# Optimization experiments

Measured on AMD Instinct MI355X. Metric: run time of the kernel, lower is better.

## Reference

```python
import jax, jax.numpy as jnp
import numpy as np

KS = 5          # kernel_size
D = 2           # spatial dim
DX = 0.01       # region kernel spacing
SCALE = 1.0
NX, NY = 32, 32
N = NX * NY


def _region_kernel():
    # gaussians.region_kernel: KS x KS grid of offsets spaced DX, centered at 0
    off = (jnp.arange(KS, dtype=jnp.float32) - (KS - 1) / 2.0) * DX
    gx, gy = jnp.meshgrid(off, off, indexing='ij')
    return jnp.stack([gx, gy], -1).reshape(-1, D)  # (KS*KS, 2)


def _build_cov(scaling, transform):
    # Cholesky-style parameterization: L lower-triangular with diag=scaling,
    # off-diag=transform; cov = L @ L^T (d=2 closed form)
    s0, s1 = scaling[:, 0], scaling[:, 1]
    t = transform[:, 0]
    c00 = s0 * s0
    c01 = s0 * t
    c11 = t * t + s1 * s1
    return jnp.stack([jnp.stack([c00, c01], -1), jnp.stack([c01, c11], -1)], -2)


def _inv2x2(c):
    det = c[:, 0, 0] * c[:, 1, 1] - c[:, 0, 1] * c[:, 1, 0]
    inv = jnp.stack([jnp.stack([c[:, 1, 1], -c[:, 0, 1]], -1),
                     jnp.stack([-c[:, 1, 0], c[:, 0, 0]], -1)], -2)
    return inv / det[:, None, None]


def setup_inputs() -> dict:
    key = jax.random.key(0)
    ks = jax.random.split(key, 20)
    # Gaussian state: grid means as in __init__
    tx = jnp.linspace(-1.0, 1.0, NX) * SCALE
    ty = jnp.linspace(-1.0, 1.0, NY) * SCALE
    gx, gy = jnp.meshgrid(tx, ty, indexing='ij')
    means = jnp.stack([gx, gy], -1).reshape(-1, D).astype(jnp.float32)
    u = 0.1 * jax.random.normal(ks[0], (N, 1), jnp.float32)
    scaling = jnp.exp(-4.5 + 0.2 * jax.random.normal(ks[1], (N, D), jnp.float32)) * SCALE
    transform = 0.002 * jax.random.normal(ks[2], (N, 1), jnp.float32)
    opacities = 2.0 + 0.1 * jax.random.normal(ks[3], (N,), jnp.float32)
    # network weights (4 heads share the first 3 layer shapes)
    convW = 0.05 * jax.random.normal(ks[4], (4, 50, 3, KS, KS), jnp.float32)
    convb = 0.01 * jax.random.normal(ks[5], (4, 50), jnp.float32)
    embW = 0.3 * jax.random.normal(ks[6], (4, 7, 30), jnp.float32)
    embb = 0.01 * jax.random.normal(ks[7], (4, 30), jnp.float32)
    l1W = 0.1 * jax.random.normal(ks[8], (4, 80, 80), jnp.float32)
    l1b = 0.01 * jax.random.normal(ks[9], (4, 80), jnp.float32)
    outW_sol = 0.1 * jax.random.normal(ks[10], (80, 1), jnp.float32)
    outb_sol = 0.01 * jax.random.normal(ks[11], (1,), jnp.float32)
    outW_trans = 0.1 * jax.random.normal(ks[12], (80, 2), jnp.float32)
    outb_trans = 0.01 * jax.random.normal(ks[13], (2,), jnp.float32)
    outW_scale = 0.1 * jax.random.normal(ks[14], (80, 2), jnp.float32)
    outb_scale = 0.01 * jax.random.normal(ks[15], (2,), jnp.float32)
    outW_tform = 0.1 * jax.random.normal(ks[16], (80, 1), jnp.float32)
    outb_tform = 0.01 * jax.random.normal(ks[17], (1,), jnp.float32)
    return {"means": means, "u": u, "scaling": scaling, "transform": transform,
            "opacities": opacities, "convW": convW, "convb": convb,
            "embW": embW, "embb": embb, "l1W": l1W, "l1b": l1b,
            "outW_sol": outW_sol, "outb_sol": outb_sol,
            "outW_trans": outW_trans, "outb_trans": outb_trans,
            "outW_scale": outW_scale, "outb_scale": outb_scale,
            "outW_tform": outW_tform, "outb_tform": outb_tform}


def reference(means, u, scaling, transform, opacities, convW, convb, embW, embb,
              l1W, l1b, outW_sol, outb_sol, outW_trans, outb_trans,
              outW_scale, outb_scale, outW_tform, outb_tform):
    n = means.shape[0]
    cov = _build_cov(scaling, transform)          # (N,2,2)
    conics = _inv2x2(cov)                         # (N,2,2)

    # --- sampling (torch.no_grad block in original) ---
    kern = _region_kernel()                                        # (25,2)
    samples = (means[:, None, :] + kern[None]).reshape(-1, D)      # (M,2), M=N*25
    bc = jnp.all(jnp.abs(samples) < SCALE, -1).astype(means.dtype)[:, None]
    alpha = jax.nn.sigmoid(opacities)                              # (N,)
    diff = samples[:, None, :] - means[None, :, :]                 # (M,N,2)
    Cq = jnp.einsum('nij,mnj->mni', conics, diff)                  # (M,N,2)
    G = jnp.exp(-0.5 * jnp.einsum('mni,mni->mn', diff, Cq)) * alpha[None, :]  # (M,N)
    u_s = G @ u                                                    # (M,1)
    # DIFFUSION pde_rhs = trace of laplacian: sum_n G * (|C q|^2 - tr(C)) * u_n
    trC = conics[:, 0, 0] + conics[:, 1, 1]
    lap = jnp.einsum('mn,mn,nc->mc', G, (Cq ** 2).sum(-1) - trC[None, :], u)  # (M,1)
    in_samples = jax.lax.stop_gradient(jnp.concatenate([u_s, lap, bc], -1))   # (M,3)

    # (N, 25, 3) -> (N, 3, 5, 5)
    img = in_samples.reshape(n, KS * KS, -1).transpose(0, 2, 1).reshape(n, -1, KS, KS)
    in_params = jnp.concatenate([means, u, scaling, transform, opacities[:, None]], -1)  # (N,7)

    # 4 Networks: conv(5x5 -> 1x1, 50ch) + param embed(7->30) + MLP(80->80->out)
    y = jnp.tanh(jnp.einsum('ncij,kocij->kno', img, convW) + convb[:, None, :])   # (4,N,50)
    e = jnp.tanh(jnp.einsum('nf,kfg->kng', in_params, embW) + embb[:, None, :])   # (4,N,30)
    h = jnp.tanh(jnp.einsum('knf,kfg->kng', jnp.concatenate([y, e], -1), l1W)
                 + l1b[:, None, :])                                               # (4,N,80)

    deltas = h[0] @ outW_sol + outb_sol          # (N,1)
    translation = h[1] @ outW_trans + outb_trans # (N,2)
    dscale = h[2] @ outW_scale + outb_scale      # (N,2)
    dtransform = h[3] @ outW_tform + outb_tform  # (N,1)

    u_new = u + deltas
    means_new = means + translation
    scaling_new = scaling * jnp.exp(dscale)
    transform_new = transform + dtransform
    cov_new = _build_cov(scaling_new, transform_new)
    return (u_new, means_new, scaling_new, transform_new, cov_new)
```

## Files before the change

### kernel.cpp

```cpp
#include <hip/hip_runtime.h>
#include <hip/hip_bf16.h>


#define NG 1024
#define WS_GD   0
#define WS_CWT  (NG * 8)

__global__ __launch_bounds__(256) void k_prep(
    const float* __restrict__ means, const float* __restrict__ u,
    const float* __restrict__ scal,  const float* __restrict__ trans,
    const float* __restrict__ opac,  const float* __restrict__ convW,
    float* __restrict__ ws)
{
    int gid = blockIdx.x * 256 + threadIdx.x;
    if (gid < NG) {
        float gmx = means[2*gid], gmy = means[2*gid+1];
        float s0  = scal[2*gid],  s1  = scal[2*gid+1];
        float tt  = trans[gid];
        float c00 = s0*s0, c01 = s0*tt, c11 = tt*tt + s1*s1;
        float idet = 1.0f / (c00*c11 - c01*c01);
        float A = c11*idet, B = -c01*idet, C = c00*idet;
        float alpha = 1.0f / (1.0f + __expf(-opac[gid]));
        float r2 = 100.0f * (c00 + c11);
        float4* dst = (float4*)(ws + WS_GD + gid*8);
        dst[0] = make_float4(gmx, gmy, A, B);
        dst[1] = make_float4(C, A + C, alpha * u[gid], r2);
    }
    float* wt = ws + WS_CWT;
    for (int idx = gid; idx < 15000; idx += gridDim.x * 256) {
        int ko = idx / 75, j = idx - ko * 75;
        wt[j * 200 + ko] = convW[idx];
    }
}

__global__ __launch_bounds__(256) void k_fused(
    const float* __restrict__ means, const float* __restrict__ u,
    const float* __restrict__ scal, const float* __restrict__ trans,
    const float* __restrict__ opac,
    const float* __restrict__ convb,
    const float* __restrict__ embW,  const float* __restrict__ embb,
    const float* __restrict__ l1W,   const float* __restrict__ l1b,
    const float* __restrict__ oWs,  const float* __restrict__ obs,
    const float* __restrict__ oWt,  const float* __restrict__ obt,
    const float* __restrict__ oWsc, const float* __restrict__ obsc,
    const float* __restrict__ oWtf, const float* __restrict__ obtf,
    const float* __restrict__ ws,
    float* __restrict__ out)
{
    __shared__ float gcomp[NG * 8];
    __shared__ float pus[8][32];
    __shared__ float plap[8][32];
    __shared__ float simg[80];
    __shared__ float hin[4][80];
    __shared__ float hv[4][80];
    __shared__ float outs[8];
    __shared__ int   cnt;

    const int t = threadIdx.x;
    const int n = blockIdx.x;
    const float mx = means[2*n], my = means[2*n+1];

    if (t == 0) cnt = 0;
    __syncthreads();
    for (int g = t; g < NG; g += 256) {
        const float4* src = (const float4*)(ws + WS_GD + g*8);
        float4 a = src[0], b = src[1];
        float ddx = fmaxf(fabsf(a.x - mx) - 0.02f, 0.0f);
        float ddy = fmaxf(fabsf(a.y - my) - 0.02f, 0.0f);
        if (ddx*ddx + ddy*ddy <= b.w) {
            int slot = atomicAdd(&cnt, 1);
            float4* dst = (float4*)(gcomp + slot*8);
            dst[0] = a; dst[1] = b;
        }
    }
    __syncthreads();
    const int nsurv = cnt;

    {
        int s = t & 31, c = t >> 5;
        if (s < 25) {
            int si = s / 5, sj = s - si * 5;
            float sx = mx + (float)(si - 2) * 0.01f;
            float sy = my + (float)(sj - 2) * 0.01f;
            float us = 0.0f, lp = 0.0f;
            #pragma unroll 2
            for (int i = c; i < nsurv; i += 8) {
                float4 a = *(const float4*)(gcomp + i*8);
                float4 b = *(const float4*)(gcomp + i*8 + 4);
                float dx = sx - a.x, dy = sy - a.y;
                float Cq0 = a.z*dx + a.w*dy;
                float Cq1 = a.w*dx + b.x*dy;
                float q   = dx*Cq0 + dy*Cq1;
                float e   = __expf(-0.5f*q) * b.z;
                us += e;
                lp += e * (Cq0*Cq0 + Cq1*Cq1 - b.y);
            }
            pus[c][s] = us; plap[c][s] = lp;
        }
    }
    __syncthreads();

    if (t < 25) {
        float us = 0.0f, lp = 0.0f;
        #pragma unroll
        for (int c = 0; c < 8; ++c) { us += pus[c][t]; lp += plap[c][t]; }
        int si = t / 5, sj = t - si * 5;
        float sx = mx + (float)(si - 2) * 0.01f;
        float sy = my + (float)(sj - 2) * 0.01f;
        simg[t]      = us;
        simg[25 + t] = lp;
        simg[50 + t] = (fabsf(sx) < 1.0f && fabsf(sy) < 1.0f) ? 1.0f : 0.0f;
    }
    __syncthreads();

    if (t < 200) {
        const float* wt = ws + WS_CWT;
        float acc = convb[t];
        #pragma unroll 5
        for (int j = 0; j < 75; ++j) acc += simg[j] * wt[j*200 + t];
        hin[t / 50][t % 50] = tanhf(acc);
    } else {
        float inp[7] = { mx, my, u[n], scal[2*n], scal[2*n+1], trans[n], opac[n] };
        for (int idx = t - 200; idx < 120; idx += 56) {
            int k = idx / 30, g = idx - k * 30;
            float acc = embb[k * 30 + g];
            #pragma unroll
            for (int f = 0; f < 7; ++f) acc += inp[f] * embW[(k*7 + f)*30 + g];
            hin[k][50 + g] = tanhf(acc);
        }
    }
    __syncthreads();

    for (int idx = t; idx < 320; idx += 256) {
        int k = idx / 80, g = idx - k * 80;
        float acc = l1b[k * 80 + g];
        #pragma unroll 8
        for (int f = 0; f < 80; ++f)
            acc += hin[k][f] * l1W[(k*80 + f)*80 + g];
        hv[k][g] = tanhf(acc);
    }
    __syncthreads();

    if (t < 6) {
        const float* W; const float* bb; int k, j, stride;
        if (t == 0)      { W = oWs;  bb = obs;  k = 0; j = 0;     stride = 1; }
        else if (t < 3)  { W = oWt;  bb = obt;  k = 1; j = t - 1; stride = 2; }
        else if (t < 5)  { W = oWsc; bb = obsc; k = 2; j = t - 3; stride = 2; }
        else             { W = oWtf; bb = obtf; k = 3; j = 0;     stride = 1; }
        float acc = bb[j];
        #pragma unroll 8
        for (int f = 0; f < 80; ++f) acc += hv[k][f] * W[f * stride + j];
        outs[t] = acc;
    }
    __syncthreads();

    if (t == 0) {
        float uu = u[n];
        float s0 = scal[2*n], s1 = scal[2*n+1];
        float tr = trans[n];
        float u_new = uu + outs[0];
        float mxn = mx + outs[1], myn = my + outs[2];
        float s0n = s0 * expf(outs[3]);
        float s1n = s1 * expf(outs[4]);
        float tn  = tr + outs[5];
        float c00 = s0n*s0n, c01 = s0n*tn, c11 = tn*tn + s1n*s1n;
        out[n]              = u_new;
        out[1024 + 2*n]     = mxn;
        out[1024 + 2*n + 1] = myn;
        out[3072 + 2*n]     = s0n;
        out[3072 + 2*n + 1] = s1n;
        out[5120 + n]       = tn;
        out[6144 + 4*n]     = c00;
        out[6144 + 4*n + 1] = c01;
        out[6144 + 4*n + 2] = c01;
        out[6144 + 4*n + 3] = c11;
    }
}

extern "C" void kernel_launch(void* const* d_in, const int* in_sizes, int n_in,
                              void* d_out, int out_size, void* d_ws, size_t ws_size,
                              hipStream_t stream)
{
    const float* means = (const float*)d_in[0];
    const float* u     = (const float*)d_in[1];
    const float* scal  = (const float*)d_in[2];
    const float* trans = (const float*)d_in[3];
    const float* opac  = (const float*)d_in[4];
    const float* convW = (const float*)d_in[5];
    float* ws = (float*)d_ws;

    k_prep<<<dim3(64), dim3(256), 0, stream>>>(means, u, scal, trans, opac,
                                               convW, ws);
    k_fused<<<dim3(NG), dim3(256), 0, stream>>>(
        means, u, scal, trans, opac,
        (const float*)d_in[6],  (const float*)d_in[7],  (const float*)d_in[8],
        (const float*)d_in[9],  (const float*)d_in[10], (const float*)d_in[11],
        (const float*)d_in[12], (const float*)d_in[13], (const float*)d_in[14],
        (const float*)d_in[15], (const float*)d_in[16], (const float*)d_in[17],
        (const float*)d_in[18], ws, (float*)d_out);
}
```

Before: 111.2 us.

## Process two Gaussians per block sharing culling and weight loads

Each block now handles two adjacent Gaussians. Culling uses a bounding box that covers both centres, and the conv and MLP layers reuse each loaded weight for two accumulators. This halves the block count and the number of global weight reads per Gaussian. Precise tanhf and expf are replaced with __expf-based approximations. The trade-off is a larger survivor list per block and half as many blocks to fill the GPU.

```diff
diff --git a/kernel.cpp b/kernel.cpp
--- a/kernel.cpp
+++ b/kernel.cpp
@@ -5,6 +5,10 @@
 #define NG 1024
 #define WS_GD   0
 #define WS_CWT  (NG * 8)
+
+__device__ __forceinline__ float tanh_fast(float x) {
+    return 1.0f - 2.0f / (__expf(2.0f * x) + 1.0f);
+}
 
 __global__ __launch_bounds__(256) void k_prep(
     const float* __restrict__ means, const float* __restrict__ u,
@@ -48,25 +52,28 @@
     float* __restrict__ out)
 {
     __shared__ float gcomp[NG * 8];
-    __shared__ float pus[8][32];
-    __shared__ float plap[8][32];
-    __shared__ float simg[80];
-    __shared__ float hin[4][80];
-    __shared__ float hv[4][80];
-    __shared__ float outs[8];
+    __shared__ float pus[2][4][32];
+    __shared__ float plap[2][4][32];
+    __shared__ float simg[2][80];
+    __shared__ float hin[2][4][80];
+    __shared__ float hv[2][4][80];
+    __shared__ float outs[2][8];
     __shared__ int   cnt;
 
-    const int t = threadIdx.x;
-    const int n = blockIdx.x;
-    const float mx = means[2*n], my = means[2*n+1];
+    const int t  = threadIdx.x;
+    const int n0 = blockIdx.x * 2;
+    const float mx0 = means[2*n0],   my0 = means[2*n0+1];
+    const float mx1 = means[2*n0+2], my1 = means[2*n0+3];
+    const float bxmin = fminf(mx0, mx1) - 0.02f, bxmax = fmaxf(mx0, mx1) + 0.02f;
+    const float bymin = fminf(my0, my1) - 0.02f, bymax = fmaxf(my0, my1) + 0.02f;
 
     if (t == 0) cnt = 0;
     __syncthreads();
     for (int g = t; g < NG; g += 256) {
         const float4* src = (const float4*)(ws + WS_GD + g*8);
         float4 a = src[0], b = src[1];
-        float ddx = fmaxf(fabsf(a.x - mx) - 0.02f, 0.0f);
-        float ddy = fmaxf(fabsf(a.y - my) - 0.02f, 0.0f);
+        float ddx = fmaxf(fmaxf(bxmin - a.x, a.x - bxmax), 0.0f);
+        float ddy = fmaxf(fmaxf(bymin - a.y, a.y - bymax), 0.0f);
         if (ddx*ddx + ddy*ddy <= b.w) {
             int slot = atomicAdd(&cnt, 1);
             float4* dst = (float4*)(gcomp + slot*8);
@@ -77,14 +84,15 @@
     const int nsurv = cnt;
 
     {
-        int s = t & 31, c = t >> 5;
+        int c = t >> 6, lane = t & 63, l = lane >> 5, s = lane & 31;
         if (s < 25) {
             int si = s / 5, sj = s - si * 5;
-            float sx = mx + (float)(si - 2) * 0.01f;
-            float sy = my + (float)(sj - 2) * 0.01f;
+            float gx = l ? mx1 : mx0, gy = l ? my1 : my0;
+            float sx = gx + (float)(si - 2) * 0.01f;
+            float sy = gy + (float)(sj - 2) * 0.01f;
             float us = 0.0f, lp = 0.0f;
             #pragma unroll 2
-            for (int i = c; i < nsurv; i += 8) {
+            for (int i = c; i < nsurv; i += 4) {
                 float4 a = *(const float4*)(gcomp + i*8);
                 float4 b = *(const float4*)(gcomp + i*8 + 4);
                 float dx = sx - a.x, dy = sy - a.y;
@@ -95,74 +103,92 @@
                 us += e;
                 lp += e * (Cq0*Cq0 + Cq1*Cq1 - b.y);
             }
-            pus[c][s] = us; plap[c][s] = lp;
-        }
-    }
-    __syncthreads();
-
-    if (t < 25) {
+            pus[l][c][s] = us; plap[l][c][s] = lp;
+        }
+    }
+    __syncthreads();
+
+    if (t < 50) {
+        int l = t / 25, s = t - l * 25;
         float us = 0.0f, lp = 0.0f;
         #pragma unroll
-        for (int c = 0; c < 8; ++c) { us += pus[c][t]; lp += plap[c][t]; }
-        int si = t / 5, sj = t - si * 5;
-        float sx = mx + (float)(si - 2) * 0.01f;
-        float sy = my + (float)(sj - 2) * 0.01f;
-        simg[t]      = us;
-        simg[25 + t] = lp;
-        simg[50 + t] = (fabsf(sx) < 1.0f && fabsf(sy) < 1.0f) ? 1.0f : 0.0f;
+        for (int c = 0; c < 4; ++c) { us += pus[l][c][s]; lp += plap[l][c][s]; }
+        int si = s / 5, sj = s - si * 5;
+        float gx = l ? mx1 : mx0, gy = l ? my1 : my0;
+        float sx = gx + (float)(si - 2) * 0.01f;
+        float sy = gy + (float)(sj - 2) * 0.01f;
+        simg[l][s]      = us;
+        simg[l][25 + s] = lp;
+        simg[l][50 + s] = (fabsf(sx) < 1.0f && fabsf(sy) < 1.0f) ? 1.0f : 0.0f;
     }
     __syncthreads();
 
     if (t < 200) {
         const float* wt = ws + WS_CWT;
-        float acc = convb[t];
+        float a0 = convb[t], a1 = a0;
         #pragma unroll 5
-        for (int j = 0; j < 75; ++j) acc += simg[j] * wt[j*200 + t];
-        hin[t / 50][t % 50] = tanhf(acc);
+        for (int j = 0; j < 75; ++j) {
+            float w = wt[j*200 + t];
+            a0 += simg[0][j] * w;
+            a1 += simg[1][j] * w;
+        }
+        int k = t / 50, o = t - k * 50;
+        hin[0][k][o] = tanh_fast(a0);
+        hin[1][k][o] = tanh_fast(a1);
     } else {
-        float inp[7] = { mx, my, u[n], scal[2*n], scal[2*n+1], trans[n], opac[n] };
-        for (int idx = t - 200; idx < 120; idx += 56) {
-            int k = idx / 30, g = idx - k * 30;
+        for (int idx = t - 200; idx < 240; idx += 56) {
+            int l = idx / 120, rem = idx - l * 120;
+            int k = rem / 30, g = rem - k * 30;
+            int n = n0 + l;
+            float inp[7] = { means[2*n], means[2*n+1], u[n], scal[2*n],
+                             scal[2*n+1], trans[n], opac[n] };
             float acc = embb[k * 30 + g];
             #pragma unroll
             for (int f = 0; f < 7; ++f) acc += inp[f] * embW[(k*7 + f)*30 + g];
-            hin[k][50 + g] = tanhf(acc);
-        }
-    }
-    __syncthreads();
-
-    for (int idx = t; idx < 320; idx += 256) {
-        int k = idx / 80, g = idx - k * 80;
-        float acc = l1b[k * 80 + g];
+            hin[l][k][50 + g] = tanh_fast(acc);
+        }
+    }
+    __syncthreads();
+
+    for (int p = t; p < 320; p += 256) {
+        int k = p / 80, g = p - k * 80;
+        float a0 = l1b[p], a1 = a0;
         #pragma unroll 8
-        for (int f = 0; f < 80; ++f)
-            acc += hin[k][f] * l1W[(k*80 + f)*80 + g];
-        hv[k][g] = tanhf(acc);
-    }
-    __syncthreads();
-
-    if (t < 6) {
+        for (int f = 0; f < 80; ++f) {
+            float w = l1W[(k*80 + f)*80 + g];
+            a0 += hin[0][k][f] * w;
+            a1 += hin[1][k][f] * w;
+        }
+        hv[0][k][g] = tanh_fast(a0);
+        hv[1][k][g] = tanh_fast(a1);
+    }
+    __syncthreads();
+
+    if (t < 12) {
+        int l = t / 6, t6 = t - l * 6;
         const float* W; const float* bb; int k, j, stride;
-        if (t == 0)      { W = oWs;  bb = obs;  k = 0; j = 0;     stride = 1; }
-        else if (t < 3)  { W = oWt;  bb = obt;  k = 1; j = t - 1; stride = 2; }
-        else if (t < 5)  { W = oWsc; bb = obsc; k = 2; j = t - 3; stride = 2; }
-        else             { W = oWtf; bb = obtf; k = 3; j = 0;     stride = 1; }
+        if (t6 == 0)      { W = oWs;  bb = obs;  k = 0; j = 0;      stride = 1; }
+        else if (t6 < 3)  { W = oWt;  bb = obt;  k = 1; j = t6 - 1; stride = 2; }
+        else if (t6 < 5)  { W = oWsc; bb = obsc; k = 2; j = t6 - 3; stride = 2; }
+        else              { W = oWtf; bb = obtf; k = 3; j = 0;      stride = 1; }
         float acc = bb[j];
         #pragma unroll 8
-        for (int f = 0; f < 80; ++f) acc += hv[k][f] * W[f * stride + j];
-        outs[t] = acc;
-    }
-    __syncthreads();
-
-    if (t == 0) {
+        for (int f = 0; f < 80; ++f) acc += hv[l][k][f] * W[f * stride + j];
+        outs[l][t6] = acc;
+    }
+    __syncthreads();
+
+    if (t < 2) {
+        int n = n0 + t;
         float uu = u[n];
         float s0 = scal[2*n], s1 = scal[2*n+1];
         float tr = trans[n];
-        float u_new = uu + outs[0];
-        float mxn = mx + outs[1], myn = my + outs[2];
-        float s0n = s0 * expf(outs[3]);
-        float s1n = s1 * expf(outs[4]);
-        float tn  = tr + outs[5];
+        float u_new = uu + outs[t][0];
+        float mxn = (t ? mx1 : mx0) + outs[t][1];
+        float myn = (t ? my1 : my0) + outs[t][2];
+        float s0n = s0 * __expf(outs[t][3]);
+        float s1n = s1 * __expf(outs[t][4]);
+        float tn  = tr + outs[t][5];
         float c00 = s0n*s0n, c01 = s0n*tn, c11 = tn*tn + s1n*s1n;
         out[n]              = u_new;
         out[1024 + 2*n]     = mxn;
@@ -191,7 +217,7 @@
 
     k_prep<<<dim3(64), dim3(256), 0, stream>>>(means, u, scal, trans, opac,
                                                convW, ws);
-    k_fused<<<dim3(NG), dim3(256), 0, stream>>>(
+    k_fused<<<dim3(NG / 2), dim3(256), 0, stream>>>(
         means, u, scal, trans, opac,
         (const float*)d_in[6],  (const float*)d_in[7],  (const float*)d_in[8],
         (const float*)d_in[9],  (const float*)d_in[10], (const float*)d_in[11],
```

Result: faster. 108.7 us (-2.3%).
